# Performance work log

Hardware: AMD Instinct MI355X
Metric: run time of the kernel (lower is better)

Reference implementation:

```python
import jax, jax.numpy as jnp
import numpy as np

E = 8          # num_experts
K = 2          # top_k
TEMP = 1.0     # router_temp
D = 1024       # model dim
H = 4 * D      # expert hidden dim
B, T = 2, 2048


def setup_inputs() -> dict:
    key = jax.random.key(0)
    ks = jax.random.split(key, 5)
    x = jax.random.normal(ks[0], (B, T, D), jnp.float32)
    gate_w = jax.random.normal(ks[1], (D, E), jnp.float32) * 0.02
    gate_b = jnp.zeros((E,), jnp.float32)
    w1 = jax.random.normal(ks[2], (E, D, H), jnp.float32) * 0.02
    b1 = jnp.zeros((E, H), jnp.float32)
    w2 = jax.random.normal(ks[3], (E, H, D), jnp.float32) * 0.02
    b2 = jnp.zeros((E, D), jnp.float32)
    return {"x": x, "gate_w": gate_w, "gate_b": gate_b,
            "w1": w1, "b1": b1, "w2": w2, "b2": b2}


def reference(x, gate_w, gate_b, w1, b1, w2, b2):
    b, t, d = x.shape
    xf = x.reshape(-1, d)                                    # [N, D]
    logits = xf @ gate_w + gate_b                            # [N, E]
    gates = jax.nn.softmax(logits / TEMP, axis=-1)
    topk_gates, topk_idx = jax.lax.top_k(gates, K)           # [N, K]
    topk_gates = topk_gates / (topk_gates.sum(-1, keepdims=True) + 1e-9)
    # combine weight per (token, expert): sum over k slots routed to expert e
    comb = (jax.nn.one_hot(topk_idx, E, dtype=xf.dtype)
            * topk_gates[..., None]).sum(axis=1)             # [N, E]
    out = jnp.zeros_like(xf)
    for e in range(E):  # small fixed loop over experts
        h = jax.nn.gelu(xf @ w1[e] + b1[e], approximate=False)  # exact GELU (torch default)
        out = out + comb[:, e:e + 1] * (h @ w2[e] + b2[e])
    return out.reshape(b, t, d)
```

## Files before the change

kernel.cpp:

```cpp
#include <hip/hip_runtime.h>
#include <math.h>

#define NTOK 4096
#define DIM  1024
#define HID  4096
#define NEXP 8
#define NROW 8192
#define KSPLIT 2

typedef __bf16 bf16;
typedef __attribute__((ext_vector_type(8))) __bf16 bf16x8;
typedef __attribute__((ext_vector_type(4))) float floatx4;

__device__ __forceinline__ void gl_lds16(const bf16* g, bf16* l) {
    __builtin_amdgcn_global_load_lds(
        (const __attribute__((address_space(1))) void*)g,
        (__attribute__((address_space(3))) void*)l, 16, 0, 0);
}

__device__ __forceinline__ float gelu_f(float v) {
    float x  = v * 0.70710678118654752f;
    float ax = fabsf(x);
    float t  = __builtin_amdgcn_rcpf(fmaf(0.3275911f, ax, 1.0f));
    float p  = fmaf(fmaf(fmaf(fmaf(1.061405429f, t, -1.453152027f),
                              t, 1.421413741f),
                         t, -0.284496736f),
                    t, 0.254829592f);
    p *= t;
    float ex = __expf(-x * x);
    float er = fmaf(-p, ex, 1.0f);
    er = copysignf(er, v);
    return 0.5f * v * (1.0f + er);
}

__global__ void zero_k(int* __restrict__ p) {
    if (threadIdx.x < 16) p[threadIdx.x] = 0;
}

__global__ __launch_bounds__(256) void convx_k(const float* __restrict__ x,
                                               bf16* __restrict__ xb)
{
    size_t gid = (size_t)blockIdx.x * 256 + threadIdx.x;
    size_t eo = gid * 8;
    floatx4 a = *(const floatx4*)(x + eo);
    floatx4 b = *(const floatx4*)(x + eo + 4);
    bf16x8 v;
#pragma unroll
    for (int j = 0; j < 4; ++j) { v[j] = (bf16)a[j]; v[4 + j] = (bf16)b[j]; }
    *(bf16x8*)&xb[eo] = v;
}

__global__ __launch_bounds__(256) void router_k(
    const float* __restrict__ x, const float* __restrict__ gw, const float* __restrict__ gb,
    int* __restrict__ counts, int* __restrict__ tok_e, float* __restrict__ tok_g)
{
    __shared__ float gws[NEXP][DIM];
    int t = threadIdx.x;
#pragma unroll
    for (int i = 0; i < 32; ++i) {
        int g = i * 256 + t;
        gws[g & 7][g >> 3] = gw[g];
    }
    __syncthreads();

    int gid = blockIdx.x * 256 + t;
    int wv = gid >> 6, lane = gid & 63;
    const float* xr = x + (size_t)wv * DIM;
    float acc[NEXP];
#pragma unroll
    for (int e = 0; e < NEXP; ++e) acc[e] = 0.f;
#pragma unroll
    for (int j = 0; j < 16; ++j) {
        int d = lane + j * 64;
        float xv = xr[d];
#pragma unroll
        for (int e = 0; e < NEXP; ++e) acc[e] += xv * gws[e][d];
    }
#pragma unroll
    for (int off = 32; off > 0; off >>= 1) {
#pragma unroll
        for (int e = 0; e < NEXP; ++e) acc[e] += __shfl_xor(acc[e], off, 64);
    }
    if (lane == 0) {
        float lg[NEXP], m = -1e30f;
        for (int e = 0; e < NEXP; ++e) { lg[e] = acc[e] + gb[e]; m = fmaxf(m, lg[e]); }
        float p[NEXP], s = 0.f;
        for (int e = 0; e < NEXP; ++e) { p[e] = expf(lg[e] - m); s += p[e]; }
        int e0 = 0;
        for (int e = 1; e < NEXP; ++e) if (p[e] > p[e0]) e0 = e;
        int e1 = (e0 == 0) ? 1 : 0;
        for (int e = 0; e < NEXP; ++e) if (e != e0 && p[e] > p[e1]) e1 = e;
        float g0 = p[e0] / s, g1 = p[e1] / s;
        float gs = g0 + g1 + 1e-9f;
        g0 /= gs; g1 /= gs;
        tok_e[wv * 2] = e0; tok_e[wv * 2 + 1] = e1;
        tok_g[wv * 2] = g0; tok_g[wv * 2 + 1] = g1;
        atomicAdd(&counts[e0], 1);
        atomicAdd(&counts[e1], 1);
    }
}

__global__ void scan_k(const int* __restrict__ counts, int* __restrict__ base)
{
    if (threadIdx.x == 0) {
        int s = 0;
#pragma unroll
        for (int e = 0; e < NEXP; ++e) { base[e] = s; s += counts[e]; }
        base[NEXP] = s;
    }
}

__global__ __launch_bounds__(256) void scatter_k(
    const int* __restrict__ tok_e, const float* __restrict__ tok_g,
    const int* __restrict__ base, int* __restrict__ counts2,
    int* __restrict__ row_token, float* __restrict__ row_gate, int* __restrict__ tok_row)
{
    int tk = blockIdx.x * 256 + threadIdx.x;
    if (tk >= NTOK) return;
#pragma unroll
    for (int k = 0; k < 2; ++k) {
        int e = tok_e[tk * 2 + k];
        int slot = atomicAdd(&counts2[e], 1);
        int r = base[e] + slot;
        row_token[r] = tk;
        row_gate[r] = tok_g[tk * 2 + k];
        tok_row[tk * 2 + k] = r;
    }
}

__global__ __launch_bounds__(256) void transpose_k(
    const float* __restrict__ src, bf16* __restrict__ dst,
    int R, int sld, size_t soff, size_t es, size_t ed)
{
    int e = blockIdx.z;
    bf16* d = dst + (size_t)e * ed;
    __shared__ __align__(16) bf16 tile[64 * 64];
    int t = threadIdx.x;
    int r0 = blockIdx.y * 64, c0 = blockIdx.x * 64;
#pragma unroll
    for (int i = 0; i < 2; ++i) {
        int c = t + i * 256;
        int rr = c >> 3, cc = c & 7;
        size_t eo = soff + (size_t)e * es + (size_t)(r0 + rr) * sld + c0 + cc * 8;
        floatx4 a = *(const floatx4*)(src + eo);
        floatx4 b = *(const floatx4*)(src + eo + 4);
        bf16x8 v;
#pragma unroll
        for (int j = 0; j < 4; ++j) { v[j] = (bf16)a[j]; v[4 + j] = (bf16)b[j]; }
        *(bf16x8*)&tile[rr * 64 + ((cc ^ ((rr >> 3) & 7)) * 8)] = v;
    }
    __syncthreads();
#pragma unroll
    for (int i = 0; i < 2; ++i) {
        int c = t + i * 256;
        int oc = c >> 3;
        int occ = c & 7;
        bf16x8 v;
#pragma unroll
        for (int j = 0; j < 8; ++j) {
            int r = occ * 8 + j;
            int p = (oc >> 3) ^ ((r >> 3) & 7);
            v[j] = tile[r * 64 + p * 8 + (oc & 7)];
        }
        *(bf16x8*)&d[(size_t)(c0 + oc) * R + r0 + occ * 8] = v;
    }
}

__global__ __launch_bounds__(256) void gemm1_k(
    const bf16* __restrict__ xb, const bf16* __restrict__ w1t, const float* __restrict__ b1,
    const int* __restrict__ counts, const int* __restrict__ base,
    const int* __restrict__ row_token, bf16* __restrict__ hbuf, int Nc, int bias_off)
{
    const int e = blockIdx.z;
    const int cnt = counts[e];
    const int rt = blockIdx.y;
    if (rt * 128 >= cnt) return;
    const int rb = base[e] + rt * 128;
    const int rend = base[e] + cnt;
    const int n0 = blockIdx.x * 128;

    __shared__ __align__(16) bf16 As[2][128 * 32];
    __shared__ __align__(16) bf16 Bs[2][128 * 32];

    const int t = threadIdx.x;
    const int wv = t >> 6, lane = t & 63;
    const int s0 = t, s1 = t + 256;
    const int ar0 = s0 >> 2, ac0 = (s0 & 3) ^ ((s0 >> 3) & 3);
    const int ar1 = s1 >> 2, ac1 = (s1 & 3) ^ ((s1 >> 3) & 3);
    int rr0 = rb + ar0; if (rr0 > NROW - 1) rr0 = NROW - 1;
    int rr1 = rb + ar1; if (rr1 > NROW - 1) rr1 = NROW - 1;
    const bf16* ga0 = xb + (size_t)row_token[rr0] * DIM + ac0 * 8;
    const bf16* ga1 = xb + (size_t)row_token[rr1] * DIM + ac1 * 8;
    const bf16* wb = w1t + (size_t)e * Nc * DIM;
    const bf16* gb0 = wb + (size_t)(n0 + ar0) * DIM + ac0 * 8;
    const bf16* gb1 = wb + (size_t)(n0 + ar1) * DIM + ac1 * 8;
    const int off0 = wv * 512, off1 = 2048 + wv * 512;

    floatx4 acc[4][4];
#pragma unroll
    for (int i = 0; i < 4; ++i)
#pragma unroll
        for (int j = 0; j < 4; ++j) acc[i][j] = floatx4{0.f, 0.f, 0.f, 0.f};

    const int wr = (wv >> 1) * 64, wc = (wv & 1) * 64;
    const int lr = lane & 15;
    const int ck = lane >> 4;

    gl_lds16(ga0, &As[0][off0]); gl_lds16(ga1, &As[0][off1]);
    gl_lds16(gb0, &Bs[0][off0]); gl_lds16(gb1, &Bs[0][off1]);

    const int NSTEP = DIM / 32;
#pragma unroll 2
    for (int i = 0; i < NSTEP; ++i) {
        const int bc = i & 1;
        asm volatile("s_waitcnt vmcnt(0)" ::: "memory");
        __builtin_amdgcn_s_barrier();
        asm volatile("" ::: "memory");
        if (i + 1 < NSTEP) {
            const int kn = (i + 1) * 32;
            gl_lds16(ga0 + kn, &As[bc ^ 1][off0]); gl_lds16(ga1 + kn, &As[bc ^ 1][off1]);
            gl_lds16(gb0 + kn, &Bs[bc ^ 1][off0]); gl_lds16(gb1 + kn, &Bs[bc ^ 1][off1]);
        }
        bf16x8 af[4], bg[4];
#pragma unroll
        for (int q = 0; q < 4; ++q) {
            int r = wr + q * 16 + lr;
            af[q] = *(const bf16x8*)&As[bc][r * 32 + ((ck ^ ((r >> 1) & 3)) * 8)];
        }
#pragma unroll
        for (int q = 0; q < 4; ++q) {
            int r = wc + q * 16 + lr;
            bg[q] = *(const bf16x8*)&Bs[bc][r * 32 + ((ck ^ ((r >> 1) & 3)) * 8)];
        }
        __builtin_amdgcn_s_setprio(1);
#pragma unroll
        for (int mi = 0; mi < 4; ++mi)
#pragma unroll
            for (int ni = 0; ni < 4; ++ni)
                acc[mi][ni] = __builtin_amdgcn_mfma_f32_16x16x32_bf16(af[mi], bg[ni], acc[mi][ni], 0, 0, 0);
        __builtin_amdgcn_s_setprio(0);
    }

#pragma unroll
    for (int mi = 0; mi < 4; ++mi) {
#pragma unroll
        for (int r = 0; r < 4; ++r) {
            int m = wr + mi * 16 + (lane >> 4) * 4 + r;
            int gr = rb + m;
            if (gr < rend) {
#pragma unroll
                for (int ni = 0; ni < 4; ++ni) {
                    int col = n0 + wc + ni * 16 + lr;
                    float v = acc[mi][ni][r] + b1[e * HID + bias_off + col];
                    hbuf[(size_t)gr * Nc + col] = (bf16)gelu_f(v);
                }
            }
        }
    }
}

__global__ __launch_bounds__(256) void gemm2_k(
    const bf16* __restrict__ hbuf, const bf16* __restrict__ w2t,
    const int* __restrict__ counts, const int* __restrict__ base,
    float* __restrict__ ybuf, int Kc, int first)
{
    const int e  = blockIdx.z >> 1;
    const int ks = blockIdx.z & 1;
    const int cnt = counts[e];
    const int rt = blockIdx.y;
    if (rt * 128 >= cnt) return;
    const int rb = base[e] + rt * 128;
    const int rend = base[e] + cnt;
    const int n0 = blockIdx.x * 128;
    const int klen = Kc / KSPLIT;
    const int kbeg = ks * klen;

    __shared__ __align__(16) bf16 As[2][128 * 32];
    __shared__ __align__(16) bf16 Bs[2][128 * 32];

    const int t = threadIdx.x;
    const int wv = t >> 6, lane = t & 63;
    const int s0 = t, s1 = t + 256;
    const int ar0 = s0 >> 2, ac0 = (s0 & 3) ^ ((s0 >> 3) & 3);
    const int ar1 = s1 >> 2, ac1 = (s1 & 3) ^ ((s1 >> 3) & 3);
    int rr0 = rb + ar0; if (rr0 > NROW - 1) rr0 = NROW - 1;
    int rr1 = rb + ar1; if (rr1 > NROW - 1) rr1 = NROW - 1;
    const bf16* ga0 = hbuf + (size_t)rr0 * Kc + kbeg + ac0 * 8;
    const bf16* ga1 = hbuf + (size_t)rr1 * Kc + kbeg + ac1 * 8;
    const bf16* wb = w2t + (size_t)e * DIM * Kc;
    const bf16* gb0 = wb + (size_t)(n0 + ar0) * Kc + kbeg + ac0 * 8;
    const bf16* gb1 = wb + (size_t)(n0 + ar1) * Kc + kbeg + ac1 * 8;
    const int off0 = wv * 512, off1 = 2048 + wv * 512;

    floatx4 acc[4][4];
#pragma unroll
    for (int i = 0; i < 4; ++i)
#pragma unroll
        for (int j = 0; j < 4; ++j) acc[i][j] = floatx4{0.f, 0.f, 0.f, 0.f};

    const int wr = (wv >> 1) * 64, wc = (wv & 1) * 64;
    const int lr = lane & 15;
    const int ck = lane >> 4;

    gl_lds16(ga0, &As[0][off0]); gl_lds16(ga1, &As[0][off1]);
    gl_lds16(gb0, &Bs[0][off0]); gl_lds16(gb1, &Bs[0][off1]);

    const int nstep = klen >> 5;
#pragma unroll 2
    for (int i = 0; i < nstep; ++i) {
        const int bc = i & 1;
        asm volatile("s_waitcnt vmcnt(0)" ::: "memory");
        __builtin_amdgcn_s_barrier();
        asm volatile("" ::: "memory");
        if (i + 1 < nstep) {
            const int kn = (i + 1) * 32;
            gl_lds16(ga0 + kn, &As[bc ^ 1][off0]); gl_lds16(ga1 + kn, &As[bc ^ 1][off1]);
            gl_lds16(gb0 + kn, &Bs[bc ^ 1][off0]); gl_lds16(gb1 + kn, &Bs[bc ^ 1][off1]);
        }
        bf16x8 af[4], bg[4];
#pragma unroll
        for (int q = 0; q < 4; ++q) {
            int r = wr + q * 16 + lr;
            af[q] = *(const bf16x8*)&As[bc][r * 32 + ((ck ^ ((r >> 1) & 3)) * 8)];
        }
#pragma unroll
        for (int q = 0; q < 4; ++q) {
            int r = wc + q * 16 + lr;
            bg[q] = *(const bf16x8*)&Bs[bc][r * 32 + ((ck ^ ((r >> 1) & 3)) * 8)];
        }
        __builtin_amdgcn_s_setprio(1);
#pragma unroll
        for (int mi = 0; mi < 4; ++mi)
#pragma unroll
            for (int ni = 0; ni < 4; ++ni)
                acc[mi][ni] = __builtin_amdgcn_mfma_f32_16x16x32_bf16(af[mi], bg[ni], acc[mi][ni], 0, 0, 0);
        __builtin_amdgcn_s_setprio(0);
    }

    float* yb = ybuf + (size_t)ks * NROW * DIM;
#pragma unroll
    for (int mi = 0; mi < 4; ++mi) {
#pragma unroll
        for (int r = 0; r < 4; ++r) {
            int m = wr + mi * 16 + (lane >> 4) * 4 + r;
            int gr = rb + m;
            if (gr < rend) {
#pragma unroll
                for (int ni = 0; ni < 4; ++ni) {
                    int col = n0 + wc + ni * 16 + lr;
                    size_t idx = (size_t)gr * DIM + col;
                    float v = acc[mi][ni][r];
                    yb[idx] = first ? v : (yb[idx] + v);
                }
            }
        }
    }
}

__global__ __launch_bounds__(256) void combine_k(
    const float* __restrict__ ybuf, const int* __restrict__ tok_row,
    const int* __restrict__ tok_e, const float* __restrict__ tok_g,
    const float* __restrict__ b2, float* __restrict__ out)
{
    int i = blockIdx.x * 256 + threadIdx.x;
    int tk = i >> 8;
    int dc = (i & 255) * 4;
    int ra = tok_row[tk * 2], rbx = tok_row[tk * 2 + 1];
    int ea = tok_e[tk * 2],  eb = tok_e[tk * 2 + 1];
    float ga = tok_g[tk * 2], gbv = tok_g[tk * 2 + 1];
    const float* y0 = ybuf;
    const float* y1 = ybuf + (size_t)NROW * DIM;
    floatx4 a0 = *(const floatx4*)&y0[(size_t)ra * DIM + dc];
    floatx4 a1 = *(const floatx4*)&y1[(size_t)ra * DIM + dc];
    floatx4 b0 = *(const floatx4*)&y0[(size_t)rbx * DIM + dc];
    floatx4 b1v = *(const floatx4*)&y1[(size_t)rbx * DIM + dc];
    floatx4 b2a = *(const floatx4*)&b2[ea * DIM + dc];
    floatx4 b2b = *(const floatx4*)&b2[eb * DIM + dc];
    floatx4 o;
#pragma unroll
    for (int j = 0; j < 4; ++j)
        o[j] = ga * (a0[j] + a1[j] + b2a[j]) + gbv * (b0[j] + b1v[j] + b2b[j]);
    *(floatx4*)&out[(size_t)tk * DIM + dc] = o;
}

extern "C" void kernel_launch(void* const* d_in, const int* in_sizes, int n_in,
                              void* d_out, int out_size, void* d_ws, size_t ws_size,
                              hipStream_t stream)
{
    const float* x  = (const float*)d_in[0];
    const float* gw = (const float*)d_in[1];
    const float* gb = (const float*)d_in[2];
    const float* w1 = (const float*)d_in[3];
    const float* b1 = (const float*)d_in[4];
    const float* w2 = (const float*)d_in[5];
    const float* b2 = (const float*)d_in[6];
    float* out = (float*)d_out;

    char* w = (char*)d_ws;
    int*   counts  = (int*)(w + 0);
    int*   counts2 = (int*)(w + 32);
    int*   base    = (int*)(w + 64);
    int*   tok_e   = (int*)(w + 256);
    float* tok_g   = (float*)(w + 256 + 32768);
    int*   row_tok = (int*)(w + 256 + 2 * 32768);
    float* row_g   = (float*)(w + 256 + 3 * 32768);
    int*   tok_row = (int*)(w + 256 + 4 * 32768);
    size_t off = 256 + 5 * 32768;
    bf16*  xb   = (bf16*)(w + off);   off += (size_t)NTOK * DIM * 2;
    float* ybuf = (float*)(w + off);  off += (size_t)KSPLIT * NROW * DIM * 4;

    int Hc = HID;
    for (;;) {
        size_t need = off + (size_t)NEXP * Hc * DIM * 2 + (size_t)NROW * Hc * 2;
        if (need <= ws_size || Hc == 128) break;
        Hc >>= 1;
    }
    bf16* wT   = (bf16*)(w + off);  off += (size_t)NEXP * Hc * DIM * 2;
    bf16* hbuf = (bf16*)(w + off);

    zero_k<<<1, 64, 0, stream>>>(counts);
    router_k<<<NTOK / 4, 256, 0, stream>>>(x, gw, gb, counts, tok_e, tok_g);
    scan_k<<<1, 64, 0, stream>>>(counts, base);
    scatter_k<<<NTOK / 256, 256, 0, stream>>>(tok_e, tok_g, base, counts2, row_tok, row_g, tok_row);
    convx_k<<<(NTOK * DIM) / 2048, 256, 0, stream>>>(x, xb);

    const int nc = HID / Hc;
    for (int ch = 0; ch < nc; ++ch) {
        transpose_k<<<dim3(Hc / 64, DIM / 64, NEXP), 256, 0, stream>>>(
            w1, wT, DIM, HID, (size_t)ch * Hc, (size_t)DIM * HID, (size_t)Hc * DIM);
        gemm1_k<<<dim3(Hc / 128, 32, NEXP), 256, 0, stream>>>(
            xb, wT, b1, counts, base, row_tok, hbuf, Hc, ch * Hc);
        transpose_k<<<dim3(DIM / 64, Hc / 64, NEXP), 256, 0, stream>>>(
            w2, wT, Hc, DIM, (size_t)ch * Hc * DIM, (size_t)HID * DIM, (size_t)DIM * Hc);
        gemm2_k<<<dim3(DIM / 128, 32, NEXP * KSPLIT), 256, 0, stream>>>(
            hbuf, wT, counts, base, ybuf, Hc, ch == 0);
    }

    combine_k<<<NTOK, 256, 0, stream>>>(ybuf, tok_row, tok_e, tok_g, b2, out);
}
```

Measured before the change: 697.5 us.

## Triple-buffer gemm2 LDS pipeline and fuse bf16 conversion of x into router

The gemm2 kernel moves from double to triple LDS buffering, prefetching two K-steps ahead and waiting with a partial vmcnt so global loads overlap more MFMA work. Separately, the fp32-to-bf16 conversion of x is folded into the router kernel, which already reads x, removing one launch and one full read of x. The extra buffer raises LDS per block, which may reduce occupancy. The fused conversion writes scalar bf16 stores instead of vectorised ones.

```diff
diff --git a/kernel.cpp b/kernel.cpp
--- a/kernel.cpp
+++ b/kernel.cpp
@@ -37,22 +37,10 @@
     if (threadIdx.x < 16) p[threadIdx.x] = 0;
 }
 
-__global__ __launch_bounds__(256) void convx_k(const float* __restrict__ x,
-                                               bf16* __restrict__ xb)
-{
-    size_t gid = (size_t)blockIdx.x * 256 + threadIdx.x;
-    size_t eo = gid * 8;
-    floatx4 a = *(const floatx4*)(x + eo);
-    floatx4 b = *(const floatx4*)(x + eo + 4);
-    bf16x8 v;
-#pragma unroll
-    for (int j = 0; j < 4; ++j) { v[j] = (bf16)a[j]; v[4 + j] = (bf16)b[j]; }
-    *(bf16x8*)&xb[eo] = v;
-}
-
 __global__ __launch_bounds__(256) void router_k(
     const float* __restrict__ x, const float* __restrict__ gw, const float* __restrict__ gb,
-    int* __restrict__ counts, int* __restrict__ tok_e, float* __restrict__ tok_g)
+    int* __restrict__ counts, int* __restrict__ tok_e, float* __restrict__ tok_g,
+    bf16* __restrict__ xb)
 {
     __shared__ float gws[NEXP][DIM];
     int t = threadIdx.x;
@@ -66,6 +54,7 @@
     int gid = blockIdx.x * 256 + t;
     int wv = gid >> 6, lane = gid & 63;
     const float* xr = x + (size_t)wv * DIM;
+    bf16* xw = xb + (size_t)wv * DIM;
     float acc[NEXP];
 #pragma unroll
     for (int e = 0; e < NEXP; ++e) acc[e] = 0.f;
@@ -73,6 +62,7 @@
     for (int j = 0; j < 16; ++j) {
         int d = lane + j * 64;
         float xv = xr[d];
+        xw[d] = (bf16)xv;
 #pragma unroll
         for (int e = 0; e < NEXP; ++e) acc[e] += xv * gws[e][d];
     }
@@ -275,8 +265,8 @@
     const int klen = Kc / KSPLIT;
     const int kbeg = ks * klen;
 
-    __shared__ __align__(16) bf16 As[2][128 * 32];
-    __shared__ __align__(16) bf16 Bs[2][128 * 32];
+    __shared__ __align__(16) bf16 As[3][128 * 32];
+    __shared__ __align__(16) bf16 Bs[3][128 * 32];
 
     const int t = threadIdx.x;
     const int wv = t >> 6, lane = t & 63;
@@ -302,20 +292,23 @@
     const int lr = lane & 15;
     const int ck = lane >> 4;
 
-    gl_lds16(ga0, &As[0][off0]); gl_lds16(ga1, &As[0][off1]);
-    gl_lds16(gb0, &Bs[0][off0]); gl_lds16(gb1, &Bs[0][off1]);
+    gl_lds16(ga0,      &As[0][off0]); gl_lds16(ga1,      &As[0][off1]);
+    gl_lds16(gb0,      &Bs[0][off0]); gl_lds16(gb1,      &Bs[0][off1]);
+    gl_lds16(ga0 + 32, &As[1][off0]); gl_lds16(ga1 + 32, &As[1][off1]);
+    gl_lds16(gb0 + 32, &Bs[1][off0]); gl_lds16(gb1 + 32, &Bs[1][off1]);
 
     const int nstep = klen >> 5;
-#pragma unroll 2
+    int bc = 0;
     for (int i = 0; i < nstep; ++i) {
-        const int bc = i & 1;
-        asm volatile("s_waitcnt vmcnt(0)" ::: "memory");
+        if (i + 1 < nstep) asm volatile("s_waitcnt vmcnt(4)" ::: "memory");
+        else               asm volatile("s_waitcnt vmcnt(0)" ::: "memory");
         __builtin_amdgcn_s_barrier();
         asm volatile("" ::: "memory");
-        if (i + 1 < nstep) {
-            const int kn = (i + 1) * 32;
-            gl_lds16(ga0 + kn, &As[bc ^ 1][off0]); gl_lds16(ga1 + kn, &As[bc ^ 1][off1]);
-            gl_lds16(gb0 + kn, &Bs[bc ^ 1][off0]); gl_lds16(gb1 + kn, &Bs[bc ^ 1][off1]);
+        if (i + 2 < nstep) {
+            int bs = bc + 2; if (bs >= 3) bs -= 3;
+            const int kn = (i + 2) * 32;
+            gl_lds16(ga0 + kn, &As[bs][off0]); gl_lds16(ga1 + kn, &As[bs][off1]);
+            gl_lds16(gb0 + kn, &Bs[bs][off0]); gl_lds16(gb1 + kn, &Bs[bs][off1]);
         }
         bf16x8 af[4], bg[4];
 #pragma unroll
@@ -335,6 +328,7 @@
             for (int ni = 0; ni < 4; ++ni)
                 acc[mi][ni] = __builtin_amdgcn_mfma_f32_16x16x32_bf16(af[mi], bg[ni], acc[mi][ni], 0, 0, 0);
         __builtin_amdgcn_s_setprio(0);
+        bc += 1; if (bc >= 3) bc -= 3;
     }
 
     float* yb = ybuf + (size_t)ks * NROW * DIM;
@@ -419,10 +413,9 @@
     bf16* hbuf = (bf16*)(w + off);
 
     zero_k<<<1, 64, 0, stream>>>(counts);
-    router_k<<<NTOK / 4, 256, 0, stream>>>(x, gw, gb, counts, tok_e, tok_g);
+    router_k<<<NTOK / 4, 256, 0, stream>>>(x, gw, gb, counts, tok_e, tok_g, xb);
     scan_k<<<1, 64, 0, stream>>>(counts, base);
     scatter_k<<<NTOK / 256, 256, 0, stream>>>(tok_e, tok_g, base, counts2, row_tok, row_g, tok_row);
-    convx_k<<<(NTOK * DIM) / 2048, 256, 0, stream>>>(x, xb);
 
     const int nc = HID / Hc;
     for (int ch = 0; ch < nc; ++ch) {
```

Measured after the change: 694.2 us. No clear change (-0.5%).
